# Performance work log

Measured on AMD Instinct MI355X. Metric: run time of the kernel, lower is better.

The kernel has to match this reference:

```python
import jax, jax.numpy as jnp
import numpy as np

L, B, F, D = 12, 2048, 6144, 768

def setup_inputs() -> dict:
    key = jax.random.key(0)
    k1, k2, k3 = jax.random.split(key, 3)
    acts = jax.random.normal(k1, (L, B, F), dtype=jnp.float32)
    # decoder weights for target layer: stacked per source layer, [L, F, D]
    W = jax.random.normal(k2, (L, F, D), dtype=jnp.float32) * 0.02
    bias = jax.random.normal(k3, (L, D), dtype=jnp.float32) * 0.01
    return {"acts": acts, "W": W, "bias": bias, "layer_idx": 11}

def reference(acts, W, bias, layer_idx):
    # decode(): sum over src_layer <= layer_idx of Linear(a[src], W[src->tgt], b[src->tgt])
    n = layer_idx + 1  # static Python int -> static slice
    a = acts[:n]       # [n, B, F]
    w = W[:n]          # [n, F, D]
    b = bias[:n]       # [n, D]
    # fused accumulation of all per-source-layer GEMMs
    recon = jnp.einsum('lbf,lfd->bd', a, w) + jnp.sum(b, axis=0)  # [B, D]
    return recon
```

## Files before the change

kernel.cpp:

```cpp
#include <hip/hip_runtime.h>
#include <hip/hip_bf16.h>

#define NB 2048
#define NF 6144
#define ND 768
#define NT (NF / 64)

typedef __attribute__((ext_vector_type(8))) __bf16 bf16x8;
typedef __attribute__((ext_vector_type(4))) float f32x4;

__device__ __forceinline__ char* lds_addr(char* base, int row, int k) {
  const int blk = ((k >> 3) ^ (row & 7) ^ ((row >> 2) & 7)) & 7;
  return base + row * 128 + (blk << 4) + ((k & 7) << 1);
}

__global__ __launch_bounds__(256) void bias_init_kernel(
    const float* __restrict__ bias, const int* __restrict__ lidx,
    float* __restrict__ out) {
  int n = lidx[0] + 1;
  int i = blockIdx.x * 256 + threadIdx.x;
  if (i >= NB * ND) return;
  int d = i % ND;
  float s = 0.f;
  for (int l = 0; l < n; ++l) s += bias[l * ND + d];
  out[i] = s;
}

__global__ __launch_bounds__(256, 2) void gemm_kernel(
    const float* __restrict__ acts, const float* __restrict__ W,
    const int* __restrict__ lidx, float* __restrict__ out) {
  const int l = blockIdx.z;
  if (l > lidx[0]) return;

  const int brow = blockIdx.x * 128;
  const int ncol = blockIdx.y * 128;

  __shared__ char cA[128 * 128];
  __shared__ char cB[128 * 128];

  const int tid = threadIdx.x;
  const int lane = tid & 63;
  const int wid = tid >> 6;
  const int wrow = (wid >> 1) * 64;
  const int wcol = (wid & 1) * 64;

  f32x4 acc[4][4];
#pragma unroll
  for (int i = 0; i < 4; ++i)
#pragma unroll
    for (int j = 0; j < 4; ++j) acc[i][j] = (f32x4){0.f, 0.f, 0.f, 0.f};

  const int s_arow = tid >> 3;
  const int s_ak = (tid & 7) * 8;
  const int s_bd = (tid & 31) * 4;
  const int s_bk = (tid >> 5) * 8;

  const float* Aptr =
      acts + (size_t)l * NB * NF + (size_t)(brow + s_arow) * NF + s_ak;
  const float* Bptr =
      W + (size_t)l * NF * ND + (size_t)s_bk * ND + (ncol + s_bd);

  float4 av[4][2];
  float4 bv[8];

  auto LOADS = [&](int kb) {
#pragma unroll
    for (int p = 0; p < 4; ++p) {
      av[p][0] = *(const float4*)(Aptr + (size_t)(32 * p) * NF + kb);
      av[p][1] = *(const float4*)(Aptr + (size_t)(32 * p) * NF + kb + 4);
    }
#pragma unroll
    for (int j = 0; j < 8; ++j)
      bv[j] = *(const float4*)(Bptr + (size_t)(kb + j) * ND);
  };

  auto STORE = [&]() {
#pragma unroll
    for (int p = 0; p < 4; ++p) {
      bf16x8 h;
      h[0] = (__bf16)av[p][0].x; h[1] = (__bf16)av[p][0].y;
      h[2] = (__bf16)av[p][0].z; h[3] = (__bf16)av[p][0].w;
      h[4] = (__bf16)av[p][1].x; h[5] = (__bf16)av[p][1].y;
      h[6] = (__bf16)av[p][1].z; h[7] = (__bf16)av[p][1].w;
      *(bf16x8*)lds_addr(cA, s_arow + 32 * p, s_ak) = h;
    }
#pragma unroll
    for (int dd = 0; dd < 4; ++dd) {
      bf16x8 h;
#pragma unroll
      for (int j = 0; j < 8; ++j) h[j] = (__bf16)bv[j][dd];
      *(bf16x8*)lds_addr(cB, s_bd + dd, s_bk) = h;
    }
  };

  LOADS(0);

  for (int kt = 0; kt < NT; ++kt) {
    __syncthreads();
    STORE();
    if (kt + 1 < NT) LOADS((kt + 1) * 64);
    __syncthreads();

#pragma unroll
    for (int s = 0; s < 2; ++s) {
      const int kk = s * 32 + (lane >> 4) * 8;
      bf16x8 aF[4], bF[4];
#pragma unroll
      for (int mi = 0; mi < 4; ++mi)
        aF[mi] = *(const bf16x8*)lds_addr(cA, wrow + mi * 16 + (lane & 15), kk);
#pragma unroll
      for (int ni = 0; ni < 4; ++ni)
        bF[ni] = *(const bf16x8*)lds_addr(cB, wcol + ni * 16 + (lane & 15), kk);
#pragma unroll
      for (int mi = 0; mi < 4; ++mi)
#pragma unroll
        for (int ni = 0; ni < 4; ++ni)
          acc[mi][ni] = __builtin_amdgcn_mfma_f32_16x16x32_bf16(
              aF[mi], bF[ni], acc[mi][ni], 0, 0, 0);
    }
  }

  const int orow = brow + wrow + ((lane >> 4) << 2);
  const int ocol = ncol + wcol + (lane & 15);
#pragma unroll
  for (int mi = 0; mi < 4; ++mi)
#pragma unroll
    for (int ni = 0; ni < 4; ++ni)
#pragma unroll
      for (int j = 0; j < 4; ++j)
        atomicAdd(out + (size_t)(orow + mi * 16 + j) * ND + (ocol + ni * 16),
                  acc[mi][ni][j]);
}

extern "C" void kernel_launch(void* const* d_in, const int* in_sizes, int n_in,
                              void* d_out, int out_size, void* d_ws, size_t ws_size,
                              hipStream_t stream) {
  const float* acts = (const float*)d_in[0];
  const float* W    = (const float*)d_in[1];
  const float* bias = (const float*)d_in[2];
  const int*   lidx = (const int*)d_in[3];
  float* out = (float*)d_out;

  const int L = in_sizes[0] / (NB * NF);

  bias_init_kernel<<<dim3((NB * ND + 255) / 256), 256, 0, stream>>>(bias, lidx, out);
  gemm_kernel<<<dim3(NB / 128, ND / 128, L), 256, 0, stream>>>(acts, W, lidx, out);
}
```

Before: 562.4 us.

## Double-buffer LDS tiles and interleave stores with MFMA to drop one barrier

Splits shared memory into two 32KB buffers and unrolls the K loop by two, so the next tile is converted and written into the alternate LDS buffer between the MFMA substeps on the current buffer. Only one barrier per K tile remains, using an explicit lgkmcnt wait plus scheduling fences. A second register set keeps two tiles of global loads in flight. This raises register pressure (two float4 staging sets under launch_bounds(256,2)) and doubles LDS to 64KB per block, which may limit occupancy.

```diff
diff --git a/kernel.cpp b/kernel.cpp
--- a/kernel.cpp
+++ b/kernel.cpp
@@ -13,6 +13,14 @@
   const int blk = ((k >> 3) ^ (row & 7) ^ ((row >> 2) & 7)) & 7;
   return base + row * 128 + (blk << 4) + ((k & 7) << 1);
 }
+
+#define BAR()                                              \
+  do {                                                     \
+    asm volatile("s_waitcnt lgkmcnt(0)" ::: "memory");     \
+    __builtin_amdgcn_sched_barrier(0);                     \
+    __builtin_amdgcn_s_barrier();                          \
+    __builtin_amdgcn_sched_barrier(0);                     \
+  } while (0)
 
 __global__ __launch_bounds__(256) void bias_init_kernel(
     const float* __restrict__ bias, const int* __restrict__ lidx,
@@ -35,8 +43,7 @@
   const int brow = blockIdx.x * 128;
   const int ncol = blockIdx.y * 128;
 
-  __shared__ char cA[128 * 128];
-  __shared__ char cB[128 * 128];
+  __shared__ char cbuf[2][32768];
 
   const int tid = threadIdx.x;
   const int lane = tid & 63;
@@ -60,65 +67,76 @@
   const float* Bptr =
       W + (size_t)l * NF * ND + (size_t)s_bk * ND + (ncol + s_bd);
 
-  float4 av[4][2];
-  float4 bv[8];
+  float4 av0[4][2], bv0[8];
+  float4 av1[4][2], bv1[8];
 
-  auto LOADS = [&](int kb) {
-#pragma unroll
-    for (int p = 0; p < 4; ++p) {
-      av[p][0] = *(const float4*)(Aptr + (size_t)(32 * p) * NF + kb);
-      av[p][1] = *(const float4*)(Aptr + (size_t)(32 * p) * NF + kb + 4);
-    }
-#pragma unroll
-    for (int j = 0; j < 8; ++j)
-      bv[j] = *(const float4*)(Bptr + (size_t)(kb + j) * ND);
-  };
+#define LOADS(av, bv, kb)                                                 \
+  do {                                                                    \
+    _Pragma("unroll") for (int p = 0; p < 4; ++p) {                       \
+      av[p][0] = *(const float4*)(Aptr + (size_t)(32 * p) * NF + (kb));   \
+      av[p][1] = *(const float4*)(Aptr + (size_t)(32 * p) * NF + (kb) + 4); \
+    }                                                                     \
+    _Pragma("unroll") for (int j = 0; j < 8; ++j)                         \
+      bv[j] = *(const float4*)(Bptr + (size_t)((kb) + j) * ND);           \
+  } while (0)
 
-  auto STORE = [&]() {
-#pragma unroll
-    for (int p = 0; p < 4; ++p) {
-      bf16x8 h;
-      h[0] = (__bf16)av[p][0].x; h[1] = (__bf16)av[p][0].y;
-      h[2] = (__bf16)av[p][0].z; h[3] = (__bf16)av[p][0].w;
-      h[4] = (__bf16)av[p][1].x; h[5] = (__bf16)av[p][1].y;
-      h[6] = (__bf16)av[p][1].z; h[7] = (__bf16)av[p][1].w;
-      *(bf16x8*)lds_addr(cA, s_arow + 32 * p, s_ak) = h;
-    }
-#pragma unroll
-    for (int dd = 0; dd < 4; ++dd) {
-      bf16x8 h;
-#pragma unroll
-      for (int j = 0; j < 8; ++j) h[j] = (__bf16)bv[j][dd];
-      *(bf16x8*)lds_addr(cB, s_bd + dd, s_bk) = h;
-    }
-  };
+#define STORE(av, bv, buf)                                                \
+  do {                                                                    \
+    char* cA_ = cbuf[buf];                                                \
+    char* cB_ = cbuf[buf] + 16384;                                        \
+    _Pragma("unroll") for (int p = 0; p < 4; ++p) {                       \
+      bf16x8 h;                                                           \
+      h[0] = (__bf16)av[p][0].x; h[1] = (__bf16)av[p][0].y;               \
+      h[2] = (__bf16)av[p][0].z; h[3] = (__bf16)av[p][0].w;               \
+      h[4] = (__bf16)av[p][1].x; h[5] = (__bf16)av[p][1].y;               \
+      h[6] = (__bf16)av[p][1].z; h[7] = (__bf16)av[p][1].w;               \
+      *(bf16x8*)lds_addr(cA_, s_arow + 32 * p, s_ak) = h;                 \
+    }                                                                     \
+    _Pragma("unroll") for (int dd = 0; dd < 4; ++dd) {                    \
+      bf16x8 h;                                                           \
+      _Pragma("unroll") for (int j = 0; j < 8; ++j)                       \
+        h[j] = (__bf16)bv[j][dd];                                         \
+      *(bf16x8*)lds_addr(cB_, s_bd + dd, s_bk) = h;                       \
+    }                                                                     \
+  } while (0)
 
-  LOADS(0);
+#define KSTEP(buf, s)                                                     \
+  do {                                                                    \
+    char* cA_ = cbuf[buf];                                                \
+    char* cB_ = cbuf[buf] + 16384;                                        \
+    const int kk = (s)*32 + (lane >> 4) * 8;                              \
+    bf16x8 aF[4], bF[4];                                                  \
+    _Pragma("unroll") for (int mi = 0; mi < 4; ++mi)                      \
+      aF[mi] = *(const bf16x8*)lds_addr(cA_, wrow + mi * 16 + (lane & 15), kk); \
+    _Pragma("unroll") for (int ni = 0; ni < 4; ++ni)                      \
+      bF[ni] = *(const bf16x8*)lds_addr(cB_, wcol + ni * 16 + (lane & 15), kk); \
+    _Pragma("unroll") for (int mi = 0; mi < 4; ++mi)                      \
+      _Pragma("unroll") for (int ni = 0; ni < 4; ++ni)                    \
+        acc[mi][ni] = __builtin_amdgcn_mfma_f32_16x16x32_bf16(            \
+            aF[mi], bF[ni], acc[mi][ni], 0, 0, 0);                        \
+  } while (0)
 
-  for (int kt = 0; kt < NT; ++kt) {
-    __syncthreads();
-    STORE();
-    if (kt + 1 < NT) LOADS((kt + 1) * 64);
-    __syncthreads();
+  LOADS(av0, bv0, 0);
+  STORE(av0, bv0, 0);
+  LOADS(av1, bv1, 64);
 
-#pragma unroll
-    for (int s = 0; s < 2; ++s) {
-      const int kk = s * 32 + (lane >> 4) * 8;
-      bf16x8 aF[4], bF[4];
-#pragma unroll
-      for (int mi = 0; mi < 4; ++mi)
-        aF[mi] = *(const bf16x8*)lds_addr(cA, wrow + mi * 16 + (lane & 15), kk);
-#pragma unroll
-      for (int ni = 0; ni < 4; ++ni)
-        bF[ni] = *(const bf16x8*)lds_addr(cB, wcol + ni * 16 + (lane & 15), kk);
-#pragma unroll
-      for (int mi = 0; mi < 4; ++mi)
-#pragma unroll
-        for (int ni = 0; ni < 4; ++ni)
-          acc[mi][ni] = __builtin_amdgcn_mfma_f32_16x16x32_bf16(
-              aF[mi], bF[ni], acc[mi][ni], 0, 0, 0);
-    }
+  for (int u = 0; u < NT / 2; ++u) {
+    BAR();
+    KSTEP(0, 0);
+    STORE(av1, bv1, 1);
+    KSTEP(0, 1);
+    if (2 * u + 2 < NT) LOADS(av0, bv0, (2 * u + 2) * 64);
+
+    BAR();
+    KSTEP(1, 0);
+    if (2 * u + 2 < NT) STORE(av0, bv0, 0);
+    KSTEP(1, 1);
+    if (2 * u + 3 < NT) LOADS(av1, bv1, (2 * u + 3) * 64);
   }
+
+#undef LOADS
+#undef STORE
+#undef KSTEP
 
   const int orow = brow + wrow + ((lane >> 4) << 2);
   const int ocol = ncol + wcol + (lane & 15);
```

Result: slower. 1.108 ms (+97.0%).

## Double-buffer LDS tiles with two-stage global prefetch and single barrier per step

Applied to the files above, without the earlier changes.

Switches the GEMM main loop to two LDS buffers. Each step computes on the current buffer, stores the next tile into the other buffer, and issues global loads two tiles ahead, so one barrier per iteration replaces two. The aim is to overlap global load latency and LDS stores with MFMA work and to remove a sync. LDS use doubles to 64 KB per block, which may limit occupancy under launch_bounds(256,2).

```diff
diff --git a/kernel.cpp b/kernel.cpp
--- a/kernel.cpp
+++ b/kernel.cpp
@@ -13,6 +13,14 @@
   const int blk = ((k >> 3) ^ (row & 7) ^ ((row >> 2) & 7)) & 7;
   return base + row * 128 + (blk << 4) + ((k & 7) << 1);
 }
+
+#define BAR()                                              \
+  do {                                                     \
+    asm volatile("s_waitcnt lgkmcnt(0)" ::: "memory");     \
+    __builtin_amdgcn_sched_barrier(0);                     \
+    __builtin_amdgcn_s_barrier();                          \
+    __builtin_amdgcn_sched_barrier(0);                     \
+  } while (0)
 
 __global__ __launch_bounds__(256) void bias_init_kernel(
     const float* __restrict__ bias, const int* __restrict__ lidx,
@@ -35,8 +43,7 @@
   const int brow = blockIdx.x * 128;
   const int ncol = blockIdx.y * 128;
 
-  __shared__ char cA[128 * 128];
-  __shared__ char cB[128 * 128];
+  __shared__ char cbuf[2][32768];
 
   const int tid = threadIdx.x;
   const int lane = tid & 63;
@@ -74,7 +81,9 @@
       bv[j] = *(const float4*)(Bptr + (size_t)(kb + j) * ND);
   };
 
-  auto STORE = [&]() {
+  auto STORE = [&](int buf) {
+    char* cA_ = cbuf[buf];
+    char* cB_ = cbuf[buf] + 16384;
 #pragma unroll
     for (int p = 0; p < 4; ++p) {
       bf16x8 h;
@@ -82,42 +91,47 @@
       h[2] = (__bf16)av[p][0].z; h[3] = (__bf16)av[p][0].w;
       h[4] = (__bf16)av[p][1].x; h[5] = (__bf16)av[p][1].y;
       h[6] = (__bf16)av[p][1].z; h[7] = (__bf16)av[p][1].w;
-      *(bf16x8*)lds_addr(cA, s_arow + 32 * p, s_ak) = h;
+      *(bf16x8*)lds_addr(cA_, s_arow + 32 * p, s_ak) = h;
     }
 #pragma unroll
     for (int dd = 0; dd < 4; ++dd) {
       bf16x8 h;
 #pragma unroll
       for (int j = 0; j < 8; ++j) h[j] = (__bf16)bv[j][dd];
-      *(bf16x8*)lds_addr(cB, s_bd + dd, s_bk) = h;
+      *(bf16x8*)lds_addr(cB_, s_bd + dd, s_bk) = h;
     }
   };
 
-  LOADS(0);
-
-  for (int kt = 0; kt < NT; ++kt) {
-    __syncthreads();
-    STORE();
-    if (kt + 1 < NT) LOADS((kt + 1) * 64);
-    __syncthreads();
-
+  auto KSTEP = [&](int buf, int s) {
+    char* cA_ = cbuf[buf];
+    char* cB_ = cbuf[buf] + 16384;
+    const int kk = s * 32 + (lane >> 4) * 8;
+    bf16x8 aF[4], bF[4];
 #pragma unroll
-    for (int s = 0; s < 2; ++s) {
-      const int kk = s * 32 + (lane >> 4) * 8;
-      bf16x8 aF[4], bF[4];
+    for (int mi = 0; mi < 4; ++mi)
+      aF[mi] = *(const bf16x8*)lds_addr(cA_, wrow + mi * 16 + (lane & 15), kk);
 #pragma unroll
-      for (int mi = 0; mi < 4; ++mi)
-        aF[mi] = *(const bf16x8*)lds_addr(cA, wrow + mi * 16 + (lane & 15), kk);
+    for (int ni = 0; ni < 4; ++ni)
+      bF[ni] = *(const bf16x8*)lds_addr(cB_, wcol + ni * 16 + (lane & 15), kk);
+#pragma unroll
+    for (int mi = 0; mi < 4; ++mi)
 #pragma unroll
       for (int ni = 0; ni < 4; ++ni)
-        bF[ni] = *(const bf16x8*)lds_addr(cB, wcol + ni * 16 + (lane & 15), kk);
-#pragma unroll
-      for (int mi = 0; mi < 4; ++mi)
-#pragma unroll
-        for (int ni = 0; ni < 4; ++ni)
-          acc[mi][ni] = __builtin_amdgcn_mfma_f32_16x16x32_bf16(
-              aF[mi], bF[ni], acc[mi][ni], 0, 0, 0);
-    }
+        acc[mi][ni] = __builtin_amdgcn_mfma_f32_16x16x32_bf16(
+            aF[mi], bF[ni], acc[mi][ni], 0, 0, 0);
+  };
+
+  LOADS(0);
+  STORE(0);
+  LOADS(64);
+
+  for (int t = 0; t < NT; ++t) {
+    BAR();
+    const int cur = t & 1;
+    KSTEP(cur, 0);
+    KSTEP(cur, 1);
+    if (t + 1 < NT) STORE(cur ^ 1);
+    if (t + 2 < NT) LOADS((t + 2) * 64);
   }
 
   const int orow = brow + wrow + ((lane >> 4) << 2);
```

Result: faster. 511.4 us (-9.1%).
